# Optimization experiments

Hardware: AMD Instinct MI355X
Metric: run time of the kernel (lower is better)

The kernel has to match this reference:

```python
import jax, jax.numpy as jnp
import numpy as np

N_NODES = 50000
N_EDGES = 800000
D_IN = 64
D_HID = 256
BN_EPS = 1e-5


def setup_inputs() -> dict:
    key = jax.random.key(0)
    ks = jax.random.split(key, 8)
    s = 1.0 / np.sqrt(D_IN)
    sg = 1.0 / np.sqrt(D_HID)
    return {
        "xs": jax.random.normal(ks[0], (N_NODES, D_IN), jnp.float32),
        "edge_index": jax.random.randint(ks[1], (2, N_EDGES), 0, N_NODES, jnp.int64),
        "W_gcn": jax.random.normal(ks[2], (D_IN, D_HID), jnp.float32) * s,
        "b_gcn": jnp.zeros((D_HID,), jnp.float32),
        "W_lin": jax.random.normal(ks[3], (D_IN, D_HID), jnp.float32) * s,
        "b_lin": jnp.zeros((D_HID,), jnp.float32),
        "W_gate": jax.random.normal(ks[4], (D_HID, D_HID), jnp.float32) * sg,
        "b_gate": jnp.zeros((D_HID,), jnp.float32),
        "bn_gamma": jnp.ones((D_HID,), jnp.float32),
        "bn_beta": jnp.zeros((D_HID,), jnp.float32),
    }


def reference(xs, edge_index, W_gcn, b_gcn, W_lin, b_lin, W_gate, b_gate, bn_gamma, bn_beta):
    N = xs.shape[0]
    # --- GCNConv: add self loops, symmetric normalization D^-1/2 (A+I) D^-1/2 ---
    loops = jnp.arange(N, dtype=edge_index.dtype)
    src = jnp.concatenate([edge_index[0], loops])  # message sources
    dst = jnp.concatenate([edge_index[1], loops])  # aggregation targets
    deg = jax.ops.segment_sum(jnp.ones(src.shape, jnp.float32), dst, num_segments=N)
    dinv = jax.lax.rsqrt(jnp.maximum(deg, 1.0))  # deg >= 1 due to self loops
    norm = dinv[src] * dinv[dst]                 # [E+N]
    h = xs @ W_gcn                               # [N, D_HID]
    z = jax.ops.segment_sum(h[src] * norm[:, None], dst, num_segments=N) + b_gcn
    z = jnp.tanh(z)
    # --- gating + linear residual ---
    g = jax.nn.sigmoid(z @ W_gate + b_gate)
    xl = xs @ W_lin + b_lin
    out = jax.nn.relu((1.0 - g) * xl + g * z)
    # --- BatchNorm over nodes (training-mode batch statistics) ---
    mu = out.mean(axis=0)
    var = out.var(axis=0)
    out = (out - mu) * jax.lax.rsqrt(var + BN_EPS) * bn_gamma + bn_beta
    # dropout is identity in eval mode
    return out
```

## Files before the change

### kernel.cpp

```cpp
#include <hip/hip_runtime.h>
#include <math.h>

#define NN 50000
#define NE 800000
#define D_IN 64
#define D_HID 256
#define BN_EPS 1e-5f
#define ZSTR 264
#define SB 128
#define BCAP 64
#define BINCAP 8192

typedef __attribute__((ext_vector_type(8))) short short8;
typedef __attribute__((ext_vector_type(4))) float f32x4;

static __device__ __forceinline__ unsigned short f2bf(float f) {
    unsigned int u = __builtin_bit_cast(unsigned int, f);
    u += 0x7FFFu + ((u >> 16) & 1u);
    return (unsigned short)(u >> 16);
}
static __device__ __forceinline__ float bf2f(unsigned short s) {
    unsigned int u = ((unsigned int)s) << 16;
    return __builtin_bit_cast(float, u);
}
static __device__ __forceinline__ float fast_sigmoid(float x) {
    return __builtin_amdgcn_rcpf(1.0f + __expf(-x));
}
static __device__ __forceinline__ float fast_tanh(float x) {
    return 1.0f - 2.0f * __builtin_amdgcn_rcpf(__expf(2.0f * x) + 1.0f);
}

static __device__ __forceinline__ long a_addr(int i, int k) {
    return ((long)((i >> 4) * 2 + (k >> 5)) << 9) + ((((k >> 3) & 3) * 16 + (i & 15)) << 3) + (k & 7);
}

__global__ __launch_bounds__(256) void k_pre(const float* __restrict__ W_gcn,
                      const float* __restrict__ W_lin, const float* __restrict__ W_gate,
                      unsigned short* __restrict__ Wp_gcn, unsigned short* __restrict__ Wp_lin,
                      unsigned short* __restrict__ Wp_gate,
                      const int* __restrict__ eidx, int* __restrict__ bincur,
                      unsigned int* __restrict__ binbuf, int E) {
    int idx = blockIdx.x * blockDim.x + threadIdx.x;
    if (idx < 98304) {
        const float* W;
        unsigned short* Wp;
        int KC, o;
        if (idx < 16384)      { W = W_gcn;  Wp = Wp_gcn;  KC = 2; o = idx; }
        else if (idx < 32768) { W = W_lin;  Wp = Wp_lin;  KC = 2; o = idx - 16384; }
        else                  { W = W_gate; Wp = Wp_gate; KC = 8; o = idx - 32768; }
        int j = o & 7;
        int lane = (o >> 3) & 63;
        int rest = o >> 9;
        int kc = rest % KC;
        int ct = rest / KC;
        int col = ct * 16 + (lane & 15);
        int k = kc * 32 + (lane >> 4) * 8 + j;
        Wp[o] = f2bf(W[k * D_HID + col]);
    }

    int b = blockIdx.x;
    int t = threadIdx.x;
    int nbb = (E + 4095) >> 12;
    if (b < nbb) {
        __shared__ int bcnt[256];
        __shared__ int gbase[256];
        bcnt[t] = 0;
        __syncthreads();
        unsigned int pair[4][4];
        int bin[4][4], lr[4][4];
        bool val[4];
#pragma unroll
        for (int c = 0; c < 4; c++) {
            int e0 = b * 4096 + c * 1024 + t * 4;
            val[c] = e0 < E;
            if (val[c]) {
                int4 s = *(const int4*)(eidx + e0);
                int4 d = *(const int4*)(eidx + E + e0);
                int ss[4] = {s.x, s.y, s.z, s.w};
                int dd[4] = {d.x, d.y, d.z, d.w};
#pragma unroll
                for (int j = 0; j < 4; j++) {
                    int bi = dd[j] >> 8;
                    bin[c][j] = bi;
                    pair[c][j] = ((unsigned int)(dd[j] & 255) << 16) | (unsigned int)ss[j];
                    lr[c][j] = atomicAdd(&bcnt[bi], 1);
                }
            }
        }
        __syncthreads();
        if (bcnt[t] > 0) gbase[t] = atomicAdd(&bincur[t], bcnt[t]);
        __syncthreads();
#pragma unroll
        for (int c = 0; c < 4; c++)
            if (val[c]) {
#pragma unroll
                for (int j = 0; j < 4; j++) {
                    int slot = gbase[bin[c][j]] + lr[c][j];
                    if (slot < BINCAP)
                        binbuf[((long)bin[c][j] << 13) + slot] = pair[c][j];
                }
            }
    }
}

__global__ __launch_bounds__(256) void k_binfill(const unsigned int* __restrict__ binbuf,
                      const int* __restrict__ bincur,
                      unsigned short* __restrict__ csr, int* __restrict__ cnt, int n) {
    __shared__ unsigned short buck[256 * BCAP];
    __shared__ int lcnt[256];
    int b = blockIdx.x;
    int t = threadIdx.x;
    lcnt[t] = 0;
    __syncthreads();
    int tot = bincur[b];
    tot = tot < BINCAP ? tot : BINCAP;
    for (int i = t; i < tot; i += 256) {
        unsigned int p = binbuf[((long)b << 13) + i];
        int dl = p >> 16;
        int src = p & 0xFFFF;
        int r = atomicAdd(&lcnt[dl], 1);
        if (r < BCAP) buck[dl * BCAP + r] = (unsigned short)src;
    }
    __syncthreads();
    int node0 = b << 8;
    if (node0 + t < n) cnt[node0 + t] = lcnt[t];
#pragma unroll
    for (int v = 0; v < 8; v++) {
        int e = (v * 256 + t) * 8;
        int node = e >> 6;
        if (node0 + node < n)
            *(short8*)(csr + ((long)(node0 + node) << 6) + (e & 63)) = *(const short8*)(&buck[e]);
    }
}

__global__ __launch_bounds__(256) void k_prep(const float* __restrict__ xs,
                           const int* __restrict__ cnt,
                           float* __restrict__ dinv, unsigned short* __restrict__ xscaled,
                           unsigned short* __restrict__ xs_p, int n) {
    int idx = blockIdx.x * blockDim.x + threadIdx.x;
    if (idx >= n * 8) {
        if (idx < n * 8 + 8) {
            short8 zv = (short8){0, 0, 0, 0, 0, 0, 0, 0};
            *(short8*)(xscaled + (long)n * D_IN + (idx - n * 8) * 8) = zv;
        }
        return;
    }
    int i = idx >> 3;
    int sub = idx & 7;
    float dv = rsqrtf(1.0f + (float)cnt[i]);
    if (sub == 0) dinv[i] = dv;
    const float* p = xs + (long)i * D_IN + sub * 8;
    float4 f0 = *(const float4*)p;
    float4 f1 = *(const float4*)(p + 4);
    float vals[8] = {f0.x, f0.y, f0.z, f0.w, f1.x, f1.y, f1.z, f1.w};
    short8 xsc, xsb;
#pragma unroll
    for (int j = 0; j < 8; j++) {
        xsc[j] = (short)f2bf(vals[j] * dv);
        xsb[j] = (short)f2bf(vals[j]);
    }
    *(short8*)(xscaled + (long)i * D_IN + sub * 8) = xsc;
    *(short8*)(xs_p + a_addr(i, sub * 8)) = xsb;
}

__global__ __launch_bounds__(256) void k_gather(const unsigned short* __restrict__ csr,
                                                const int* __restrict__ cnt,
                                                const unsigned short* __restrict__ xscaled,
                                                const float* __restrict__ dinv,
                                                unsigned short* __restrict__ agg_p, int n) {
    int wv = threadIdx.x >> 6;
    int lane = threadIdx.x & 63;
    int sub = lane & 7;
    int grp = lane >> 3;
    int i = blockIdx.x * 4 + wv;
    if (i >= n) return;
    int c = cnt[i];
    c = c < BCAP ? c : BCAP;
    float acc[8];
#pragma unroll
    for (int j = 0; j < 8; j++) acc[j] = 0.f;
    {
        int m = c;
        int idxv = (lane < m) ? (int)csr[i * BCAP + lane] : 0;
        int tmax = (m + 7) >> 3;
        for (int t = 0; t < tmax; t++) {
            int e = t * 8 + grp;
            int rowv = __shfl(idxv, e);
            int row = (e < m) ? rowv : n;
            short8 v = *(const short8*)(xscaled + (long)row * D_IN + sub * 8);
#pragma unroll
            for (int j = 0; j < 8; j++) acc[j] += bf2f((unsigned short)v[j]);
        }
    }
#pragma unroll
    for (int d = 8; d <= 32; d <<= 1)
#pragma unroll
        for (int j = 0; j < 8; j++) acc[j] += __shfl_xor(acc[j], d);
    if (grp == 0) {
        float dv = dinv[i];
        short8 sv = *(const short8*)(xscaled + (long)i * D_IN + sub * 8);
        short8 o;
#pragma unroll
        for (int j = 0; j < 8; j++)
            o[j] = (short)f2bf((acc[j] + bf2f((unsigned short)sv[j])) * dv);
        *(short8*)(agg_p + a_addr(i, sub * 8)) = o;
    }
}

__global__ __launch_bounds__(256, 4) void k_fused(const unsigned short* __restrict__ agg_p,
                        const unsigned short* __restrict__ xs_p,
                        const unsigned short* __restrict__ Wp_gcn,
                        const unsigned short* __restrict__ Wp_lin,
                        const unsigned short* __restrict__ Wp_gate,
                        const float* __restrict__ b_gcn,
                        const float* __restrict__ bg,
                        const float* __restrict__ bl,
                        unsigned short* __restrict__ out_pre,
                        int n) {
    __shared__ unsigned short z_lds[32 * ZSTR];

    int tid = threadIdx.x;
    int wv = tid >> 6;
    int lane = tid & 63;
    int l15 = lane & 15;
    int quad = lane >> 4;
    int rt0 = blockIdx.x * 2;

    short8 aggf[2][2], xsf[2][2];
#pragma unroll
    for (int r = 0; r < 2; r++)
#pragma unroll
        for (int kc = 0; kc < 2; kc++) {
            aggf[r][kc] = *(const short8*)(agg_p + ((long)((rt0 + r) * 2 + kc) << 9) + lane * 8);
            xsf[r][kc]  = *(const short8*)(xs_p  + ((long)((rt0 + r) * 2 + kc) << 9) + lane * 8);
        }

    {
        short8 wg[2][4];
#pragma unroll
        for (int kc = 0; kc < 2; kc++)
#pragma unroll
            for (int tn = 0; tn < 4; tn++)
                wg[kc][tn] = *(const short8*)(Wp_gcn + ((long)((wv * 4 + tn) * 2 + kc) << 9) + lane * 8);
        float bias[4];
#pragma unroll
        for (int tn = 0; tn < 4; tn++) bias[tn] = b_gcn[wv * 64 + tn * 16 + l15];
#pragma unroll
        for (int r = 0; r < 2; r++) {
            f32x4 accz[4];
#pragma unroll
            for (int c = 0; c < 4; c++) accz[c] = (f32x4){0.f, 0.f, 0.f, 0.f};
#pragma unroll
            for (int kc = 0; kc < 2; kc++)
#pragma unroll
                for (int tn = 0; tn < 4; tn++)
                    accz[tn] = __builtin_amdgcn_mfma_f32_16x16x32_bf16(aggf[r][kc], wg[kc][tn], accz[tn], 0, 0, 0);
#pragma unroll
            for (int tn = 0; tn < 4; tn++) {
                int col = wv * 64 + tn * 16 + l15;
#pragma unroll
                for (int r2 = 0; r2 < 4; r2++)
                    z_lds[(r * 16 + quad * 4 + r2) * ZSTR + col] = f2bf(fast_tanh(accz[tn][r2] + bias[tn]));
            }
        }
    }
    __syncthreads();

    uint2 o_pk[2][4];
    float bgc[4], blc[4];
#pragma unroll
    for (int tn = 0; tn < 4; tn++) {
        int col = wv * 64 + tn * 16 + l15;
        bgc[tn] = bg[col];
        blc[tn] = bl[col];
    }
#pragma unroll
    for (int tnp = 0; tnp < 2; tnp++) {
        f32x4 accl[2][2];
#pragma unroll
        for (int r = 0; r < 2; r++)
#pragma unroll
            for (int h = 0; h < 2; h++) accl[r][h] = (f32x4){0.f, 0.f, 0.f, 0.f};
#pragma unroll
        for (int kc = 0; kc < 2; kc++) {
            short8 wl0 = *(const short8*)(Wp_lin + ((long)((wv * 4 + tnp * 2 + 0) * 2 + kc) << 9) + lane * 8);
            short8 wl1 = *(const short8*)(Wp_lin + ((long)((wv * 4 + tnp * 2 + 1) * 2 + kc) << 9) + lane * 8);
#pragma unroll
            for (int r = 0; r < 2; r++) {
                accl[r][0] = __builtin_amdgcn_mfma_f32_16x16x32_bf16(xsf[r][kc], wl0, accl[r][0], 0, 0, 0);
                accl[r][1] = __builtin_amdgcn_mfma_f32_16x16x32_bf16(xsf[r][kc], wl1, accl[r][1], 0, 0, 0);
            }
        }
        f32x4 acc1[2][2];
#pragma unroll
        for (int r = 0; r < 2; r++)
#pragma unroll
            for (int h = 0; h < 2; h++) acc1[r][h] = (f32x4){0.f, 0.f, 0.f, 0.f};
#pragma unroll
        for (int kc = 0; kc < 8; kc++) {
            short8 w0 = *(const short8*)(Wp_gate + ((long)((wv * 4 + tnp * 2 + 0) * 8 + kc) << 9) + lane * 8);
            short8 w1 = *(const short8*)(Wp_gate + ((long)((wv * 4 + tnp * 2 + 1) * 8 + kc) << 9) + lane * 8);
#pragma unroll
            for (int r = 0; r < 2; r++) {
                short8 af = *(const short8*)(&z_lds[(r * 16 + l15) * ZSTR + kc * 32 + quad * 8]);
                acc1[r][0] = __builtin_amdgcn_mfma_f32_16x16x32_bf16(af, w0, acc1[r][0], 0, 0, 0);
                acc1[r][1] = __builtin_amdgcn_mfma_f32_16x16x32_bf16(af, w1, acc1[r][1], 0, 0, 0);
            }
        }
#pragma unroll
        for (int h = 0; h < 2; h++) {
            int tn = tnp * 2 + h;
            int col = wv * 64 + tn * 16 + l15;
#pragma unroll
            for (int r = 0; r < 2; r++) {
                unsigned short op4[4];
#pragma unroll
                for (int r2 = 0; r2 < 4; r2++) {
                    int rl = r * 16 + quad * 4 + r2;
                    float g = fast_sigmoid(acc1[r][h][r2] + bgc[tn]);
                    float zv = bf2f(z_lds[rl * ZSTR + col]);
                    float xv = accl[r][h][r2] + blc[tn];
                    float o = fmaxf((1.f - g) * xv + g * zv, 0.f);
                    op4[r2] = f2bf(o);
                }
                o_pk[r][tn].x = (unsigned int)op4[0] | ((unsigned int)op4[1] << 16);
                o_pk[r][tn].y = (unsigned int)op4[2] | ((unsigned int)op4[3] << 16);
            }
        }
    }
    __syncthreads();

#pragma unroll
    for (int r = 0; r < 2; r++)
#pragma unroll
        for (int tn = 0; tn < 4; tn++) {
            int col = wv * 64 + tn * 16 + l15;
            int rl = r * 16 + quad * 4;
            z_lds[(rl + 0) * ZSTR + col] = (unsigned short)(o_pk[r][tn].x & 0xFFFF);
            z_lds[(rl + 1) * ZSTR + col] = (unsigned short)(o_pk[r][tn].x >> 16);
            z_lds[(rl + 2) * ZSTR + col] = (unsigned short)(o_pk[r][tn].y & 0xFFFF);
            z_lds[(rl + 3) * ZSTR + col] = (unsigned short)(o_pk[r][tn].y >> 16);
        }
    __syncthreads();

#pragma unroll
    for (int it = 0; it < 4; it++) {
        int g = it * 2048 + tid * 8;
        int row = g >> 8;
        int col = g & 255;
        short8 v = *(const short8*)(&z_lds[row * ZSTR + col]);
        *(short8*)(out_pre + (long)(blockIdx.x * 32 + row) * D_HID + col) = v;
    }
    (void)n;
}

__global__ __launch_bounds__(256) void k_stats(const unsigned short* __restrict__ op,
                        float* __restrict__ colsum, float* __restrict__ colsumsq, int n) {
    __shared__ float reds[4][32][8];
    __shared__ float redq[4][32][8];
    int tid = threadIdx.x;
    int wv = tid >> 6;
    int lane = tid & 63;
    int cg = tid & 31;
    int rb = tid >> 5;
    float ls[8], lq[8];
#pragma unroll
    for (int j = 0; j < 8; j++) { ls[j] = 0.f; lq[j] = 0.f; }
    for (int row = blockIdx.x * 8 + rb; row < n; row += SB * 8) {
        short8 v = *(const short8*)(op + (long)row * D_HID + cg * 8);
#pragma unroll
        for (int j = 0; j < 8; j++) {
            float f = bf2f((unsigned short)v[j]);
            ls[j] += f;
            lq[j] += f * f;
        }
    }
#pragma unroll
    for (int j = 0; j < 8; j++) {
        ls[j] += __shfl_xor(ls[j], 32);
        lq[j] += __shfl_xor(lq[j], 32);
    }
    if (lane < 32) {
#pragma unroll
        for (int j = 0; j < 8; j++) {
            reds[wv][cg][j] = ls[j];
            redq[wv][cg][j] = lq[j];
        }
    }
    __syncthreads();
    if (wv == 0 && lane < 32) {
#pragma unroll
        for (int j = 0; j < 8; j++) {
            float s = reds[0][cg][j] + reds[1][cg][j] + reds[2][cg][j] + reds[3][cg][j];
            float q = redq[0][cg][j] + redq[1][cg][j] + redq[2][cg][j] + redq[3][cg][j];
            atomicAdd(&colsum[cg * 8 + j], s);
            atomicAdd(&colsumsq[cg * 8 + j], q);
        }
    }
}

__global__ __launch_bounds__(256) void k_bn_apply(const unsigned short* __restrict__ op,
                           float* __restrict__ out,
                           const float* __restrict__ colsum, const float* __restrict__ colsumsq,
                           const float* __restrict__ gamma, const float* __restrict__ beta,
                           int n, int total8) {
    int i8 = blockIdx.x * blockDim.x + threadIdx.x;
    if (i8 >= total8) return;
    long idx = (long)i8 * 8;
    short8 p = *(const short8*)(op + idx);
    int c = (int)(idx & (D_HID - 1));
    float inv_n = 1.0f / (float)n;
    float vo[8];
#pragma unroll
    for (int j = 0; j < 8; j++) {
        float mu = colsum[c + j] * inv_n;
        float var = colsumsq[c + j] * inv_n - mu * mu;
        float sc = gamma[c + j] * rsqrtf(var + BN_EPS);
        vo[j] = bf2f((unsigned short)p[j]) * sc + (beta[c + j] - mu * sc);
    }
    float4 v0 = {vo[0], vo[1], vo[2], vo[3]};
    float4 v1 = {vo[4], vo[5], vo[6], vo[7]};
    *(float4*)(out + idx) = v0;
    *(float4*)(out + idx + 4) = v1;
}

extern "C" void kernel_launch(void* const* d_in, const int* in_sizes, int n_in,
                              void* d_out, int out_size, void* d_ws, size_t ws_size,
                              hipStream_t stream) {
    const float* xs     = (const float*)d_in[0];
    const int*   eidx   = (const int*)d_in[1];
    const float* W_gcn  = (const float*)d_in[2];
    const float* b_gcn  = (const float*)d_in[3];
    const float* W_lin  = (const float*)d_in[4];
    const float* b_lin  = (const float*)d_in[5];
    const float* W_gate = (const float*)d_in[6];
    const float* b_gate = (const float*)d_in[7];
    const float* gamma  = (const float*)d_in[8];
    const float* beta   = (const float*)d_in[9];
    float* out = (float*)d_out;

    const int n = in_sizes[0] / D_IN;
    const int E = in_sizes[1] / 2;
    const int npad = (n + 63) & ~63;
    const int nbins = (n + 255) >> 8;

    char* ws = (char*)d_ws;
    size_t off = 0;
    auto alloc = [&](size_t bytes) {
        char* p = ws + off;
        off += (bytes + 511) & ~(size_t)511;
        return p;
    };
    size_t zero_begin = off;
    int*            bincur   = (int*)alloc(256 * 4);
    float*          colsum   = (float*)alloc(D_HID * 4);
    float*          colsumsq = (float*)alloc(D_HID * 4);
    size_t zero_end = off;
    int*            cnt      = (int*)alloc((size_t)n * 4);
    unsigned int*   binbuf   = (unsigned int*)alloc((size_t)nbins * BINCAP * 4);
    unsigned short* csr      = (unsigned short*)alloc((size_t)n * BCAP * 2);
    float*          dinv     = (float*)alloc((size_t)n * 4);
    unsigned short* xscaled  = (unsigned short*)alloc((size_t)(n + 1) * D_IN * 2);
    unsigned short* xs_p     = (unsigned short*)alloc((size_t)npad * D_IN * 2);
    unsigned short* agg_p    = (unsigned short*)alloc((size_t)npad * D_IN * 2);
    unsigned short* out_pre  = (unsigned short*)alloc((size_t)npad * D_HID * 2);
    unsigned short* Wp_gcn   = (unsigned short*)alloc((size_t)D_IN * D_HID * 2);
    unsigned short* Wp_lin   = (unsigned short*)alloc((size_t)D_IN * D_HID * 2);
    unsigned short* Wp_gate  = (unsigned short*)alloc((size_t)D_HID * D_HID * 2);
    (void)ws_size;

    const int B = 256;

    hipMemsetAsync(ws + zero_begin, 0, zero_end - zero_begin, stream);
    k_pre<<<384, B, 0, stream>>>(W_gcn, W_lin, W_gate, Wp_gcn, Wp_lin, Wp_gate,
                                 eidx, bincur, binbuf, E);
    k_binfill<<<nbins, B, 0, stream>>>(binbuf, bincur, csr, cnt, n);
    k_prep<<<(n * 8 + 8 + B - 1) / B, B, 0, stream>>>(xs, cnt, dinv, xscaled, xs_p, n);
    k_gather<<<(n + 3) / 4, B, 0, stream>>>(csr, cnt, xscaled, dinv, agg_p, n);
    k_fused<<<npad / 32, B, 0, stream>>>(agg_p, xs_p, Wp_gcn, Wp_lin, Wp_gate,
                                         b_gcn, b_gate, b_lin, out_pre, n);
    k_stats<<<SB, B, 0, stream>>>(out_pre, colsum, colsumsq, n);
    {
        int total8 = n * D_HID / 8;
        k_bn_apply<<<(total8 + B - 1) / B, B, 0, stream>>>(out_pre, out, colsum, colsumsq,
                                                           gamma, beta, n, total8);
    }
}
```

Baseline: 214.5 us.

## Split gather features into two 32-column planes and add nontemporal loads/stores

```diff
diff --git a/kernel.cpp b/kernel.cpp
--- a/kernel.cpp
+++ b/kernel.cpp
@@ -13,6 +13,8 @@
 
 typedef __attribute__((ext_vector_type(8))) short short8;
 typedef __attribute__((ext_vector_type(4))) float f32x4;
+typedef __attribute__((ext_vector_type(4))) int int4v;
+typedef __attribute__((ext_vector_type(4))) float float4v;
 
 static __device__ __forceinline__ unsigned short f2bf(float f) {
     unsigned int u = __builtin_bit_cast(unsigned int, f);
@@ -74,10 +76,10 @@
             int e0 = b * 4096 + c * 1024 + t * 4;
             val[c] = e0 < E;
             if (val[c]) {
-                int4 s = *(const int4*)(eidx + e0);
-                int4 d = *(const int4*)(eidx + E + e0);
-                int ss[4] = {s.x, s.y, s.z, s.w};
-                int dd[4] = {d.x, d.y, d.z, d.w};
+                int4v s = __builtin_nontemporal_load((const int4v*)(eidx + e0));
+                int4v d = __builtin_nontemporal_load((const int4v*)(eidx + E + e0));
+                int ss[4] = {s[0], s[1], s[2], s[3]};
+                int dd[4] = {d[0], d[1], d[2], d[3]};
 #pragma unroll
                 for (int j = 0; j < 4; j++) {
                     int bi = dd[j] >> 8;
@@ -135,13 +137,15 @@
 
 __global__ __launch_bounds__(256) void k_prep(const float* __restrict__ xs,
                            const int* __restrict__ cnt,
-                           float* __restrict__ dinv, unsigned short* __restrict__ xscaled,
+                           float* __restrict__ dinv, unsigned short* __restrict__ xpl,
                            unsigned short* __restrict__ xs_p, int n) {
+    long PS = (long)(n + 1) * 32;
     int idx = blockIdx.x * blockDim.x + threadIdx.x;
     if (idx >= n * 8) {
         if (idx < n * 8 + 8) {
+            int sub = idx - n * 8;
             short8 zv = (short8){0, 0, 0, 0, 0, 0, 0, 0};
-            *(short8*)(xscaled + (long)n * D_IN + (idx - n * 8) * 8) = zv;
+            *(short8*)(xpl + (long)(sub >> 2) * PS + (long)n * 32 + (sub & 3) * 8) = zv;
         }
         return;
     }
@@ -150,28 +154,29 @@
     float dv = rsqrtf(1.0f + (float)cnt[i]);
     if (sub == 0) dinv[i] = dv;
     const float* p = xs + (long)i * D_IN + sub * 8;
-    float4 f0 = *(const float4*)p;
-    float4 f1 = *(const float4*)(p + 4);
-    float vals[8] = {f0.x, f0.y, f0.z, f0.w, f1.x, f1.y, f1.z, f1.w};
+    float4v f0 = __builtin_nontemporal_load((const float4v*)p);
+    float4v f1 = __builtin_nontemporal_load((const float4v*)(p + 4));
+    float vals[8] = {f0[0], f0[1], f0[2], f0[3], f1[0], f1[1], f1[2], f1[3]};
     short8 xsc, xsb;
 #pragma unroll
     for (int j = 0; j < 8; j++) {
         xsc[j] = (short)f2bf(vals[j] * dv);
         xsb[j] = (short)f2bf(vals[j]);
     }
-    *(short8*)(xscaled + (long)i * D_IN + sub * 8) = xsc;
+    *(short8*)(xpl + (long)(sub >> 2) * PS + (long)i * 32 + (sub & 3) * 8) = xsc;
     *(short8*)(xs_p + a_addr(i, sub * 8)) = xsb;
 }
 
 __global__ __launch_bounds__(256) void k_gather(const unsigned short* __restrict__ csr,
                                                 const int* __restrict__ cnt,
-                                                const unsigned short* __restrict__ xscaled,
+                                                const unsigned short* __restrict__ xpl_p,
                                                 const float* __restrict__ dinv,
-                                                unsigned short* __restrict__ agg_p, int n) {
+                                                unsigned short* __restrict__ agg_p,
+                                                int n, int p) {
     int wv = threadIdx.x >> 6;
     int lane = threadIdx.x & 63;
-    int sub = lane & 7;
-    int grp = lane >> 3;
+    int sub = lane & 3;
+    int grp = lane >> 2;
     int i = blockIdx.x * 4 + wv;
     if (i >= n) return;
     int c = cnt[i];
@@ -179,31 +184,28 @@
     float acc[8];
 #pragma unroll
     for (int j = 0; j < 8; j++) acc[j] = 0.f;
-    {
-        int m = c;
-        int idxv = (lane < m) ? (int)csr[i * BCAP + lane] : 0;
-        int tmax = (m + 7) >> 3;
-        for (int t = 0; t < tmax; t++) {
-            int e = t * 8 + grp;
-            int rowv = __shfl(idxv, e);
-            int row = (e < m) ? rowv : n;
-            short8 v = *(const short8*)(xscaled + (long)row * D_IN + sub * 8);
-#pragma unroll
-            for (int j = 0; j < 8; j++) acc[j] += bf2f((unsigned short)v[j]);
-        }
-    }
-#pragma unroll
-    for (int d = 8; d <= 32; d <<= 1)
+    int idxv = (lane < c) ? (int)__builtin_nontemporal_load(csr + ((long)i << 6) + lane) : 0;
+    int tmax = (c + 15) >> 4;
+    for (int t = 0; t < tmax; t++) {
+        int e = t * 16 + grp;
+        int rowv = __shfl(idxv, e);
+        int row = (e < c) ? rowv : n;
+        short8 v = *(const short8*)(xpl_p + (long)row * 32 + sub * 8);
+#pragma unroll
+        for (int j = 0; j < 8; j++) acc[j] += bf2f((unsigned short)v[j]);
+    }
+#pragma unroll
+    for (int d = 4; d <= 32; d <<= 1)
 #pragma unroll
         for (int j = 0; j < 8; j++) acc[j] += __shfl_xor(acc[j], d);
-    if (grp == 0) {
+    if (lane < 4) {
         float dv = dinv[i];
-        short8 sv = *(const short8*)(xscaled + (long)i * D_IN + sub * 8);
+        short8 sv = *(const short8*)(xpl_p + (long)i * 32 + sub * 8);
         short8 o;
 #pragma unroll
         for (int j = 0; j < 8; j++)
             o[j] = (short)f2bf((acc[j] + bf2f((unsigned short)sv[j])) * dv);
-        *(short8*)(agg_p + a_addr(i, sub * 8)) = o;
+        *(short8*)(agg_p + ((long)((i >> 4) * 2 + p) << 9) + (sub * 16 + (i & 15)) * 8) = o;
     }
 }
 
@@ -418,10 +420,10 @@
         float sc = gamma[c + j] * rsqrtf(var + BN_EPS);
         vo[j] = bf2f((unsigned short)p[j]) * sc + (beta[c + j] - mu * sc);
     }
-    float4 v0 = {vo[0], vo[1], vo[2], vo[3]};
-    float4 v1 = {vo[4], vo[5], vo[6], vo[7]};
-    *(float4*)(out + idx) = v0;
-    *(float4*)(out + idx + 4) = v1;
+    float4v v0 = {vo[0], vo[1], vo[2], vo[3]};
+    float4v v1 = {vo[4], vo[5], vo[6], vo[7]};
+    __builtin_nontemporal_store(v0, (float4v*)(out + idx));
+    __builtin_nontemporal_store(v1, (float4v*)(out + idx + 4));
 }
 
 extern "C" void kernel_launch(void* const* d_in, const int* in_sizes, int n_in,
@@ -443,6 +445,7 @@
     const int E = in_sizes[1] / 2;
     const int npad = (n + 63) & ~63;
     const int nbins = (n + 255) >> 8;
+    const long PS = (long)(n + 1) * 32;
 
     char* ws = (char*)d_ws;
     size_t off = 0;
@@ -460,7 +463,7 @@
     unsigned int*   binbuf   = (unsigned int*)alloc((size_t)nbins * BINCAP * 4);
     unsigned short* csr      = (unsigned short*)alloc((size_t)n * BCAP * 2);
     float*          dinv     = (float*)alloc((size_t)n * 4);
-    unsigned short* xscaled  = (unsigned short*)alloc((size_t)(n + 1) * D_IN * 2);
+    unsigned short* xpl      = (unsigned short*)alloc((size_t)2 * PS * 2);
     unsigned short* xs_p     = (unsigned short*)alloc((size_t)npad * D_IN * 2);
     unsigned short* agg_p    = (unsigned short*)alloc((size_t)npad * D_IN * 2);
     unsigned short* out_pre  = (unsigned short*)alloc((size_t)npad * D_HID * 2);
@@ -475,8 +478,9 @@
     k_pre<<<384, B, 0, stream>>>(W_gcn, W_lin, W_gate, Wp_gcn, Wp_lin, Wp_gate,
                                  eidx, bincur, binbuf, E);
     k_binfill<<<nbins, B, 0, stream>>>(binbuf, bincur, csr, cnt, n);
-    k_prep<<<(n * 8 + 8 + B - 1) / B, B, 0, stream>>>(xs, cnt, dinv, xscaled, xs_p, n);
-    k_gather<<<(n + 3) / 4, B, 0, stream>>>(csr, cnt, xscaled, dinv, agg_p, n);
+    k_prep<<<(n * 8 + 8 + B - 1) / B, B, 0, stream>>>(xs, cnt, dinv, xpl, xs_p, n);
+    k_gather<<<(n + 3) / 4, B, 0, stream>>>(csr, cnt, xpl,          dinv, agg_p, n, 0);
+    k_gather<<<(n + 3) / 4, B, 0, stream>>>(csr, cnt, xpl + PS,     dinv, agg_p, n, 1);
     k_fused<<<npad / 32, B, 0, stream>>>(agg_p, xs_p, Wp_gcn, Wp_lin, Wp_gate,
                                          b_gcn, b_gate, b_lin, out_pre, n);
     k_stats<<<SB, B, 0, stream>>>(out_pre, colsum, colsumsq, n);
```

Result: slower. 231.8 us (+8.1%).
